# Kernel optimization log

Hardware: AMD Instinct MI355X
Metric: run time of the kernel (lower is better)

## Reference

```python
import jax, jax.numpy as jnp
import numpy as np

C_Z = 128
C_HIDDEN = 128
N_RES = 384
B = 1
EPS = 1e-5


def _layernorm(x, w, b):
    mu = jnp.mean(x, axis=-1, keepdims=True)
    var = jnp.mean(jnp.square(x - mu), axis=-1, keepdims=True)
    return (x - mu) * jax.lax.rsqrt(var + EPS) * w + b


def setup_inputs() -> dict:
    key = jax.random.key(0)
    ks = jax.random.split(key, 16)
    s_z = 1.0 / np.sqrt(C_Z)
    s_h = 1.0 / np.sqrt(C_HIDDEN)
    return {
        "z": jax.random.normal(ks[0], (B, N_RES, N_RES, C_Z), dtype=jnp.float32),
        "mask": jnp.ones((B, N_RES, N_RES), dtype=jnp.float32),
        "ln_in_w": jnp.ones((C_Z,), jnp.float32),
        "ln_in_b": jnp.zeros((C_Z,), jnp.float32),
        "a_g_w": jax.random.normal(ks[1], (C_HIDDEN, C_Z), jnp.float32) * s_z,
        "a_g_b": jnp.zeros((C_HIDDEN,), jnp.float32),
        "a_p_w": jax.random.normal(ks[2], (C_HIDDEN, C_Z), jnp.float32) * s_z,
        "a_p_b": jnp.zeros((C_HIDDEN,), jnp.float32),
        "b_g_w": jax.random.normal(ks[3], (C_HIDDEN, C_Z), jnp.float32) * s_z,
        "b_g_b": jnp.zeros((C_HIDDEN,), jnp.float32),
        "b_p_w": jax.random.normal(ks[4], (C_HIDDEN, C_Z), jnp.float32) * s_z,
        "b_p_b": jnp.zeros((C_HIDDEN,), jnp.float32),
        "g_w": jax.random.normal(ks[5], (C_Z, C_Z), jnp.float32) * s_z,
        "g_b": jnp.zeros((C_Z,), jnp.float32),
        "ln_out_w": jnp.ones((C_HIDDEN,), jnp.float32),
        "ln_out_b": jnp.zeros((C_HIDDEN,), jnp.float32),
        "z_w": jax.random.normal(ks[6], (C_Z, C_HIDDEN), jnp.float32) * s_h,
        "z_b": jnp.zeros((C_Z,), jnp.float32),
    }


def reference(z, mask, ln_in_w, ln_in_b, a_g_w, a_g_b, a_p_w, a_p_b,
              b_g_w, b_g_b, b_p_w, b_p_b, g_w, g_b,
              ln_out_w, ln_out_b, z_w, z_b):
    # z: [B, N, N, c_z]; mask: [B, N, N]
    m = mask[..., None]
    zn = _layernorm(z, ln_in_w, ln_in_b)
    # gated projections (fused LN+GEMM+sigmoid*mul in the Triton kernel)
    a = m * jax.nn.sigmoid(jnp.einsum("bijc,hc->bijh", zn, a_g_w) + a_g_b) \
          * (jnp.einsum("bijc,hc->bijh", zn, a_p_w) + a_p_b)
    b = m * jax.nn.sigmoid(jnp.einsum("bijc,hc->bijh", zn, b_g_w) + b_g_b) \
          * (jnp.einsum("bijc,hc->bijh", zn, b_p_w) + b_p_b)
    # outgoing triangle update: contract over third node k, per channel
    x = jnp.einsum("bikh,bjkh->bijh", a, b)
    # output path: sigmoid(gate(zn)) * linear_z(LN_out(x))
    xn = _layernorm(x, ln_out_w, ln_out_b)
    gate = jax.nn.sigmoid(jnp.einsum("bijc,oc->bijo", zn, g_w) + g_b)
    out = gate * (jnp.einsum("bijh,oh->bijo", xn, z_w) + z_b)
    return out
```

## Files before the change

kernel.cpp:

```cpp
#include <hip/hip_runtime.h>

#define NRES 384
#define CD   128
#define MTOT (NRES*NRES)

typedef unsigned short u16;
typedef __bf16 bf16x8 __attribute__((ext_vector_type(8)));
typedef float  f32x16 __attribute__((ext_vector_type(16)));

static __device__ __forceinline__ u16 f2bf(float f) {
  __bf16 b = (__bf16)f;
  return __builtin_bit_cast(u16, b);
}
static __device__ __forceinline__ float bf2f(u16 v) {
  return __uint_as_float(((unsigned)v) << 16);
}
static __device__ __forceinline__ float sigmoidf(float x) {
  return 1.0f / (1.0f + __expf(-x));
}

__global__ void k_cvt_w(const float* w0, const float* w1, const float* w2,
                        const float* w3, const float* w4, const float* w5,
                        u16* wb) {
  int i = blockIdx.x * 256 + threadIdx.x;
  const float* srcs[6] = {w0, w1, w2, w3, w4, w5};
  wb[i] = f2bf(srcs[i >> 14][i & 16383]);
}

__global__ __launch_bounds__(256) void k_ln_in(const float* __restrict__ z,
                                               const float* __restrict__ w,
                                               const float* __restrict__ b,
                                               u16* __restrict__ zn) {
  int wv = threadIdx.x >> 6, lane = threadIdx.x & 63;
  float2 wv2 = ((const float2*)w)[lane];
  float2 bv2 = ((const float2*)b)[lane];
  for (int rr = 0; rr < 4; ++rr) {
    size_t row = (size_t)blockIdx.x * 16 + wv * 4 + rr;
    float2 v = ((const float2*)(z + row * CD))[lane];
    float s = v.x + v.y;
#pragma unroll
    for (int off = 32; off >= 1; off >>= 1) s += __shfl_xor(s, off);
    float mu = s * (1.0f / CD);
    float dx = v.x - mu, dy = v.y - mu;
    float vr = dx * dx + dy * dy;
#pragma unroll
    for (int off = 32; off >= 1; off >>= 1) vr += __shfl_xor(vr, off);
    float rs = rsqrtf(vr * (1.0f / CD) + 1e-5f);
    ushort2 o;
    o.x = f2bf(dx * rs * wv2.x + bv2.x);
    o.y = f2bf(dy * rs * wv2.y + bv2.y);
    ((ushort2*)(zn + row * CD))[lane] = o;
  }
}

__global__ __launch_bounds__(256) void k_proj(
    const u16* __restrict__ zn, const float* __restrict__ mask,
    const u16* __restrict__ wb,
    const float* __restrict__ agb, const float* __restrict__ apb,
    const float* __restrict__ bgb, const float* __restrict__ bpb,
    const float* __restrict__ gb,
    u16* __restrict__ a_out, u16* __restrict__ b_out, u16* __restrict__ gate_out) {
  int type = blockIdx.y;
  int m0   = blockIdx.x * 64;
  int wv = threadIdx.x >> 6, lane = threadIdx.x & 63;
  int nl = lane & 31, s = lane >> 5;
  int h = wv * 32 + nl;

  const u16 *wgp, *wpp = nullptr;
  const float *bgp, *bpp = nullptr;
  if (type == 0)      { wgp = wb;          wpp = wb + 16384; bgp = agb; bpp = apb; }
  else if (type == 1) { wgp = wb + 32768;  wpp = wb + 49152; bgp = bgb; bpp = bpb; }
  else                { wgp = wb + 65536;                    bgp = gb; }

  __shared__ u16 znt[64][136];

#pragma unroll
  for (int it = 0; it < 4; ++it) {
    int idx = it * 256 + threadIdx.x;
    int r = idx >> 4, c8 = idx & 15;
    *(uint4*)&znt[r][c8 * 8] =
        *(const uint4*)(zn + (size_t)(m0 + r) * CD + c8 * 8);
  }

  bf16x8 wgf[8], wpf[8];
#pragma unroll
  for (int kk = 0; kk < 8; ++kk) {
    wgf[kk] = *(const bf16x8*)(wgp + h * CD + kk * 16 + s * 8);
    if (type < 2) wpf[kk] = *(const bf16x8*)(wpp + h * CD + kk * 16 + s * 8);
  }
  __syncthreads();

  if (type < 2) {
    f32x16 accg[2], accp[2];
#pragma unroll
    for (int i = 0; i < 16; ++i) { accg[0][i] = 0; accg[1][i] = 0; accp[0][i] = 0; accp[1][i] = 0; }
#pragma unroll
    for (int kk = 0; kk < 8; ++kk) {
      bf16x8 zf0 = *(const bf16x8*)&znt[nl][kk * 16 + s * 8];
      bf16x8 zf1 = *(const bf16x8*)&znt[32 + nl][kk * 16 + s * 8];
      accg[0] = __builtin_amdgcn_mfma_f32_32x32x16_bf16(wgf[kk], zf0, accg[0], 0, 0, 0);
      accg[1] = __builtin_amdgcn_mfma_f32_32x32x16_bf16(wgf[kk], zf1, accg[1], 0, 0, 0);
      accp[0] = __builtin_amdgcn_mfma_f32_32x32x16_bf16(wpf[kk], zf0, accp[0], 0, 0, 0);
      accp[1] = __builtin_amdgcn_mfma_f32_32x32x16_bf16(wpf[kk], zf1, accp[1], 0, 0, 0);
    }
    float mk0 = mask[m0 + nl];
    float mk1 = mask[m0 + 32 + nl];
    u16* outp = (type == 0) ? a_out : b_out;
#pragma unroll
    for (int r = 0; r < 16; ++r) {
      int hh = wv * 32 + (r & 3) + 8 * (r >> 2) + 4 * s;
      float bg = bgp[hh], bp = bpp[hh];
      u16* rowp = outp + (size_t)hh * MTOT + m0 + nl;
      rowp[0]  = f2bf(mk0 * sigmoidf(accg[0][r] + bg) * (accp[0][r] + bp));
      rowp[32] = f2bf(mk1 * sigmoidf(accg[1][r] + bg) * (accp[1][r] + bp));
    }
  } else {
    f32x16 accg[2];
#pragma unroll
    for (int i = 0; i < 16; ++i) { accg[0][i] = 0; accg[1][i] = 0; }
#pragma unroll
    for (int kk = 0; kk < 8; ++kk) {
      bf16x8 zf0 = *(const bf16x8*)&znt[nl][kk * 16 + s * 8];
      bf16x8 zf1 = *(const bf16x8*)&znt[32 + nl][kk * 16 + s * 8];
      accg[0] = __builtin_amdgcn_mfma_f32_32x32x16_bf16(zf0, wgf[kk], accg[0], 0, 0, 0);
      accg[1] = __builtin_amdgcn_mfma_f32_32x32x16_bf16(zf1, wgf[kk], accg[1], 0, 0, 0);
    }
    float bgv = bgp[h];
#pragma unroll
    for (int ms = 0; ms < 2; ++ms)
#pragma unroll
      for (int r = 0; r < 16; ++r) {
        int rowoff = (r & 3) + 8 * (r >> 2) + 4 * s;
        int mg = m0 + ms * 32 + rowoff;
        gate_out[(size_t)mg * CD + h] = f2bf(sigmoidf(accg[ms][r] + bgv));
      }
  }
}

__global__ __launch_bounds__(256) void k_tri(const u16* __restrict__ a,
                                             const u16* __restrict__ b,
                                             u16* __restrict__ x) {
  int h  = blockIdx.y;
  int tm = blockIdx.x / 3, tn = blockIdx.x % 3;
  int i0 = tm * 128, j0 = tn * 128;
  const u16* ah = a + (size_t)h * MTOT;
  const u16* bh = b + (size_t)h * MTOT;

  __shared__ u16 At[128][72];
  __shared__ u16 Bt[128][72];

  int wv = threadIdx.x >> 6, lane = threadIdx.x & 63;
  int nl = lane & 31, s = lane >> 5;
  int wr = wv >> 1, wc = wv & 1;

  f32x16 acc[4];
#pragma unroll
  for (int q = 0; q < 4; ++q)
#pragma unroll
    for (int i = 0; i < 16; ++i) acc[q][i] = 0;

  for (int k0 = 0; k0 < NRES; k0 += 64) {
#pragma unroll
    for (int it = 0; it < 4; ++it) {
      int idx = it * 256 + threadIdx.x;
      int r = idx >> 3, c8 = idx & 7;
      *(uint4*)&At[r][c8 * 8] =
          *(const uint4*)(ah + (size_t)(i0 + r) * NRES + k0 + c8 * 8);
    }
#pragma unroll
    for (int it = 0; it < 4; ++it) {
      int idx = it * 256 + threadIdx.x;
      int r = idx >> 3, c8 = idx & 7;
      *(uint4*)&Bt[r][c8 * 8] =
          *(const uint4*)(bh + (size_t)(j0 + r) * NRES + k0 + c8 * 8);
    }
    __syncthreads();
#pragma unroll
    for (int kk = 0; kk < 4; ++kk) {
      bf16x8 af0 = *(const bf16x8*)&At[wr * 64 + nl][kk * 16 + s * 8];
      bf16x8 af1 = *(const bf16x8*)&At[wr * 64 + 32 + nl][kk * 16 + s * 8];
      bf16x8 bf0 = *(const bf16x8*)&Bt[wc * 64 + nl][kk * 16 + s * 8];
      bf16x8 bf1 = *(const bf16x8*)&Bt[wc * 64 + 32 + nl][kk * 16 + s * 8];
      acc[0] = __builtin_amdgcn_mfma_f32_32x32x16_bf16(af0, bf0, acc[0], 0, 0, 0);
      acc[1] = __builtin_amdgcn_mfma_f32_32x32x16_bf16(af0, bf1, acc[1], 0, 0, 0);
      acc[2] = __builtin_amdgcn_mfma_f32_32x32x16_bf16(af1, bf0, acc[2], 0, 0, 0);
      acc[3] = __builtin_amdgcn_mfma_f32_32x32x16_bf16(af1, bf1, acc[3], 0, 0, 0);
    }
    __syncthreads();
  }

  u16* xh = x + (size_t)h * MTOT;
#pragma unroll
  for (int msub = 0; msub < 2; ++msub)
#pragma unroll
    for (int nsub = 0; nsub < 2; ++nsub) {
      int j = j0 + wc * 64 + nsub * 32 + nl;
#pragma unroll
      for (int r = 0; r < 16; ++r) {
        int i = i0 + wr * 64 + msub * 32 + (r & 3) + 8 * (r >> 2) + 4 * s;
        xh[(size_t)i * NRES + j] = f2bf(acc[msub * 2 + nsub][r]);
      }
    }
}

__global__ __launch_bounds__(256) void k_out(
    const u16* __restrict__ x, const u16* __restrict__ gate,
    const u16* __restrict__ wb,
    const float* __restrict__ lnw, const float* __restrict__ lnb,
    const float* __restrict__ zb, float* __restrict__ out) {
  int m0 = blockIdx.x * 64;
  int t = threadIdx.x;
  int wv = t >> 6, lane = t & 63, nl = lane & 31, s = lane >> 5;
  int o = wv * 32 + nl;

  __shared__ u16 xnt[64][136];

  const u16* zwp = wb + 5 * 16384;
  bf16x8 zwf[8];
#pragma unroll
  for (int kk = 0; kk < 8; ++kk)
    zwf[kk] = *(const bf16x8*)(zwp + o * CD + kk * 16 + s * 8);

#pragma unroll
  for (int ps = 0; ps < 2; ++ps) {
    int idx = ps * 256 + t;
    int hp = idx >> 3, mc = idx & 7;
    uint4 v0 = *(const uint4*)(x + (size_t)(2 * hp)     * MTOT + m0 + mc * 8);
    uint4 v1 = *(const uint4*)(x + (size_t)(2 * hp + 1) * MTOT + m0 + mc * 8);
    unsigned c0[4] = {v0.x, v0.y, v0.z, v0.w};
    unsigned c1[4] = {v1.x, v1.y, v1.z, v1.w};
#pragma unroll
    for (int q = 0; q < 4; ++q) {
      ushort2 lo, hi;
      lo.x = (u16)(c0[q] & 0xffffu); lo.y = (u16)(c1[q] & 0xffffu);
      hi.x = (u16)(c0[q] >> 16);     hi.y = (u16)(c1[q] >> 16);
      *(ushort2*)&xnt[mc * 8 + 2 * q][2 * hp]     = lo;
      *(ushort2*)&xnt[mc * 8 + 2 * q + 1][2 * hp] = hi;
    }
  }
  __syncthreads();

  int r = t >> 2, q = t & 3;
  float vals[32];
  float sum = 0;
#pragma unroll
  for (int j = 0; j < 32; ++j) { float v = bf2f(xnt[r][q * 32 + j]); vals[j] = v; sum += v; }
  sum += __shfl_xor(sum, 1);
  sum += __shfl_xor(sum, 2);
  float mu = sum * (1.0f / CD);
  float var = 0;
#pragma unroll
  for (int j = 0; j < 32; ++j) { float d = vals[j] - mu; var += d * d; }
  var += __shfl_xor(var, 1);
  var += __shfl_xor(var, 2);
  float rs = rsqrtf(var * (1.0f / CD) + 1e-5f);
#pragma unroll
  for (int j = 0; j < 32; ++j) {
    int hh = q * 32 + j;
    xnt[r][hh] = f2bf((vals[j] - mu) * rs * lnw[hh] + lnb[hh]);
  }
  __syncthreads();

  f32x16 acc[2];
#pragma unroll
  for (int i = 0; i < 16; ++i) { acc[0][i] = 0; acc[1][i] = 0; }
#pragma unroll
  for (int kk = 0; kk < 8; ++kk) {
    bf16x8 af0 = *(const bf16x8*)&xnt[nl][kk * 16 + s * 8];
    bf16x8 af1 = *(const bf16x8*)&xnt[32 + nl][kk * 16 + s * 8];
    acc[0] = __builtin_amdgcn_mfma_f32_32x32x16_bf16(af0, zwf[kk], acc[0], 0, 0, 0);
    acc[1] = __builtin_amdgcn_mfma_f32_32x32x16_bf16(af1, zwf[kk], acc[1], 0, 0, 0);
  }

  float zbv = zb[o];
#pragma unroll
  for (int ms = 0; ms < 2; ++ms)
#pragma unroll
    for (int rr = 0; rr < 16; ++rr) {
      int rowoff = (rr & 3) + 8 * (rr >> 2) + 4 * s;
      int mg = m0 + ms * 32 + rowoff;
      float g = bf2f(gate[(size_t)mg * CD + o]);
      out[(size_t)mg * CD + o] = g * (acc[ms][rr] + zbv);
    }
}

extern "C" void kernel_launch(void* const* d_in, const int* in_sizes, int n_in,
                              void* d_out, int out_size, void* d_ws, size_t ws_size,
                              hipStream_t stream) {
  const float* z       = (const float*)d_in[0];
  const float* mask    = (const float*)d_in[1];
  const float* ln_in_w = (const float*)d_in[2];
  const float* ln_in_b = (const float*)d_in[3];
  const float* a_g_w   = (const float*)d_in[4];
  const float* a_g_b   = (const float*)d_in[5];
  const float* a_p_w   = (const float*)d_in[6];
  const float* a_p_b   = (const float*)d_in[7];
  const float* b_g_w   = (const float*)d_in[8];
  const float* b_g_b   = (const float*)d_in[9];
  const float* b_p_w   = (const float*)d_in[10];
  const float* b_p_b   = (const float*)d_in[11];
  const float* g_w     = (const float*)d_in[12];
  const float* g_b     = (const float*)d_in[13];
  const float* ln_o_w  = (const float*)d_in[14];
  const float* ln_o_b  = (const float*)d_in[15];
  const float* z_w     = (const float*)d_in[16];
  const float* z_b     = (const float*)d_in[17];
  float* out = (float*)d_out;

  const size_t SZ = (size_t)MTOT * CD * sizeof(u16);
  char* w = (char*)d_ws;
  u16* zn   = (u16*)(w);
  u16* a    = (u16*)(w + SZ);
  u16* b    = (u16*)(w + 2 * SZ);
  u16* gate = (u16*)(w + 3 * SZ);
  u16* wb   = (u16*)(w + 4 * SZ);
  (void)ws_size; (void)in_sizes; (void)n_in; (void)out_size;

  k_cvt_w<<<384, 256, 0, stream>>>(a_g_w, a_p_w, b_g_w, b_p_w, g_w, z_w, wb);
  k_ln_in<<<MTOT / 16, 256, 0, stream>>>(z, ln_in_w, ln_in_b, zn);
  k_proj<<<dim3(MTOT / 64, 3), 256, 0, stream>>>(zn, mask, wb,
      a_g_b, a_p_b, b_g_b, b_p_b, g_b, a, b, gate);
  k_tri<<<dim3(9, 128), 256, 0, stream>>>(a, b, zn);
  k_out<<<MTOT / 64, 256, 0, stream>>>(zn, gate, wb, ln_o_w, ln_o_b, z_b, out);
}
```

Measured before the change: 316.1 us.

## Use direct global-to-LDS loads with XOR swizzle and double-buffered projection tiles

k_proj now covers four 64-row tiles per block, reusing the weight fragments held in registers. It double-buffers the zn tile in LDS, loading it with global_load_lds so the next tile's fetch overlaps the current MFMA work. k_tri also switches to global_load_lds with an XOR-swizzled, unpadded LDS layout in place of the register round-trip and padding. The intent is less VGPR staging traffic, fewer LDS bank conflicts and amortised weight loads. The cost is a quarter as many k_proj blocks, and synchronisation correctness now depends on the asynchronous LDS loads having completed before each barrier.

```diff
diff --git a/kernel.cpp b/kernel.cpp
--- a/kernel.cpp
+++ b/kernel.cpp
@@ -17,6 +17,12 @@
 }
 static __device__ __forceinline__ float sigmoidf(float x) {
   return 1.0f / (1.0f + __expf(-x));
+}
+
+static __device__ __forceinline__ void gl16(const void* g, void* l) {
+  __builtin_amdgcn_global_load_lds(
+      (const __attribute__((address_space(1))) void*)g,
+      (__attribute__((address_space(3))) void*)l, 16, 0, 0);
 }
 
 __global__ void k_cvt_w(const float* w0, const float* w1, const float* w2,
@@ -61,10 +67,11 @@
     const float* __restrict__ gb,
     u16* __restrict__ a_out, u16* __restrict__ b_out, u16* __restrict__ gate_out) {
   int type = blockIdx.y;
-  int m0   = blockIdx.x * 64;
-  int wv = threadIdx.x >> 6, lane = threadIdx.x & 63;
+  int m_base = blockIdx.x * 256;
+  int lane = threadIdx.x & 63;
+  int wvu = __builtin_amdgcn_readfirstlane(threadIdx.x >> 6);
   int nl = lane & 31, s = lane >> 5;
-  int h = wv * 32 + nl;
+  int h = wvu * 32 + nl;
 
   const u16 *wgp, *wpp = nullptr;
   const float *bgp, *bpp = nullptr;
@@ -72,15 +79,7 @@
   else if (type == 1) { wgp = wb + 32768;  wpp = wb + 49152; bgp = bgb; bpp = bpb; }
   else                { wgp = wb + 65536;                    bgp = gb; }
 
-  __shared__ u16 znt[64][136];
-
-#pragma unroll
-  for (int it = 0; it < 4; ++it) {
-    int idx = it * 256 + threadIdx.x;
-    int r = idx >> 4, c8 = idx & 15;
-    *(uint4*)&znt[r][c8 * 8] =
-        *(const uint4*)(zn + (size_t)(m0 + r) * CD + c8 * 8);
-  }
+  __shared__ u16 znt[2][64][128];
 
   bf16x8 wgf[8], wpf[8];
 #pragma unroll
@@ -88,53 +87,77 @@
     wgf[kk] = *(const bf16x8*)(wgp + h * CD + kk * 16 + s * 8);
     if (type < 2) wpf[kk] = *(const bf16x8*)(wpp + h * CD + kk * 16 + s * 8);
   }
+
+  int rl = lane >> 4, p16 = lane & 15;
+#define STAGE_ZNT(mt, bf)                                                   \
+  {                                                                         \
+    _Pragma("unroll")                                                       \
+    for (int j = 0; j < 4; ++j) {                                           \
+      int row = wvu * 16 + j * 4 + rl;                                      \
+      int gc = (p16 ^ (row & 7)) << 3;                                      \
+      gl16(zn + (size_t)((mt) + row) * CD + gc, &znt[bf][wvu * 16 + j * 4][0]); \
+    }                                                                       \
+  }
+
+  STAGE_ZNT(m_base, 0);
   __syncthreads();
 
-  if (type < 2) {
-    f32x16 accg[2], accp[2];
-#pragma unroll
-    for (int i = 0; i < 16; ++i) { accg[0][i] = 0; accg[1][i] = 0; accp[0][i] = 0; accp[1][i] = 0; }
-#pragma unroll
-    for (int kk = 0; kk < 8; ++kk) {
-      bf16x8 zf0 = *(const bf16x8*)&znt[nl][kk * 16 + s * 8];
-      bf16x8 zf1 = *(const bf16x8*)&znt[32 + nl][kk * 16 + s * 8];
-      accg[0] = __builtin_amdgcn_mfma_f32_32x32x16_bf16(wgf[kk], zf0, accg[0], 0, 0, 0);
-      accg[1] = __builtin_amdgcn_mfma_f32_32x32x16_bf16(wgf[kk], zf1, accg[1], 0, 0, 0);
-      accp[0] = __builtin_amdgcn_mfma_f32_32x32x16_bf16(wpf[kk], zf0, accp[0], 0, 0, 0);
-      accp[1] = __builtin_amdgcn_mfma_f32_32x32x16_bf16(wpf[kk], zf1, accp[1], 0, 0, 0);
-    }
-    float mk0 = mask[m0 + nl];
-    float mk1 = mask[m0 + 32 + nl];
-    u16* outp = (type == 0) ? a_out : b_out;
-#pragma unroll
-    for (int r = 0; r < 16; ++r) {
-      int hh = wv * 32 + (r & 3) + 8 * (r >> 2) + 4 * s;
-      float bg = bgp[hh], bp = bpp[hh];
-      u16* rowp = outp + (size_t)hh * MTOT + m0 + nl;
-      rowp[0]  = f2bf(mk0 * sigmoidf(accg[0][r] + bg) * (accp[0][r] + bp));
-      rowp[32] = f2bf(mk1 * sigmoidf(accg[1][r] + bg) * (accp[1][r] + bp));
-    }
-  } else {
-    f32x16 accg[2];
-#pragma unroll
-    for (int i = 0; i < 16; ++i) { accg[0][i] = 0; accg[1][i] = 0; }
-#pragma unroll
-    for (int kk = 0; kk < 8; ++kk) {
-      bf16x8 zf0 = *(const bf16x8*)&znt[nl][kk * 16 + s * 8];
-      bf16x8 zf1 = *(const bf16x8*)&znt[32 + nl][kk * 16 + s * 8];
-      accg[0] = __builtin_amdgcn_mfma_f32_32x32x16_bf16(zf0, wgf[kk], accg[0], 0, 0, 0);
-      accg[1] = __builtin_amdgcn_mfma_f32_32x32x16_bf16(zf1, wgf[kk], accg[1], 0, 0, 0);
-    }
-    float bgv = bgp[h];
-#pragma unroll
-    for (int ms = 0; ms < 2; ++ms)
+  for (int ms = 0; ms < 4; ++ms) {
+    int cur = ms & 1;
+    if (ms < 3) STAGE_ZNT(m_base + (ms + 1) * 64, cur ^ 1);
+    int mt = m_base + ms * 64;
+
+    if (type < 2) {
+      f32x16 accg[2], accp[2];
+#pragma unroll
+      for (int i = 0; i < 16; ++i) { accg[0][i] = 0; accg[1][i] = 0; accp[0][i] = 0; accp[1][i] = 0; }
+#pragma unroll
+      for (int kk = 0; kk < 8; ++kk) {
+        int c = ((kk * 2 + s) ^ (nl & 7)) << 3;
+        bf16x8 zf0 = *(const bf16x8*)&znt[cur][nl][c];
+        bf16x8 zf1 = *(const bf16x8*)&znt[cur][32 + nl][c];
+        accg[0] = __builtin_amdgcn_mfma_f32_32x32x16_bf16(wgf[kk], zf0, accg[0], 0, 0, 0);
+        accg[1] = __builtin_amdgcn_mfma_f32_32x32x16_bf16(wgf[kk], zf1, accg[1], 0, 0, 0);
+        accp[0] = __builtin_amdgcn_mfma_f32_32x32x16_bf16(wpf[kk], zf0, accp[0], 0, 0, 0);
+        accp[1] = __builtin_amdgcn_mfma_f32_32x32x16_bf16(wpf[kk], zf1, accp[1], 0, 0, 0);
+      }
+      __syncthreads();
+      float mk0 = mask[mt + nl];
+      float mk1 = mask[mt + 32 + nl];
+      u16* outp = (type == 0) ? a_out : b_out;
 #pragma unroll
       for (int r = 0; r < 16; ++r) {
-        int rowoff = (r & 3) + 8 * (r >> 2) + 4 * s;
-        int mg = m0 + ms * 32 + rowoff;
-        gate_out[(size_t)mg * CD + h] = f2bf(sigmoidf(accg[ms][r] + bgv));
+        int hh = wvu * 32 + (r & 3) + 8 * (r >> 2) + 4 * s;
+        float bg = bgp[hh], bp = bpp[hh];
+        u16* rowp = outp + (size_t)hh * MTOT + mt + nl;
+        rowp[0]  = f2bf(mk0 * sigmoidf(accg[0][r] + bg) * (accp[0][r] + bp));
+        rowp[32] = f2bf(mk1 * sigmoidf(accg[1][r] + bg) * (accp[1][r] + bp));
       }
-  }
+    } else {
+      f32x16 accg[2];
+#pragma unroll
+      for (int i = 0; i < 16; ++i) { accg[0][i] = 0; accg[1][i] = 0; }
+#pragma unroll
+      for (int kk = 0; kk < 8; ++kk) {
+        int c = ((kk * 2 + s) ^ (nl & 7)) << 3;
+        bf16x8 zf0 = *(const bf16x8*)&znt[cur][nl][c];
+        bf16x8 zf1 = *(const bf16x8*)&znt[cur][32 + nl][c];
+        accg[0] = __builtin_amdgcn_mfma_f32_32x32x16_bf16(zf0, wgf[kk], accg[0], 0, 0, 0);
+        accg[1] = __builtin_amdgcn_mfma_f32_32x32x16_bf16(zf1, wgf[kk], accg[1], 0, 0, 0);
+      }
+      __syncthreads();
+      float bgv = bgp[h];
+#pragma unroll
+      for (int msb = 0; msb < 2; ++msb)
+#pragma unroll
+        for (int r = 0; r < 16; ++r) {
+          int rowoff = (r & 3) + 8 * (r >> 2) + 4 * s;
+          int mg = mt + msb * 32 + rowoff;
+          gate_out[(size_t)mg * CD + h] = f2bf(sigmoidf(accg[msb][r] + bgv));
+        }
+    }
+  }
+#undef STAGE_ZNT
 }
 
 __global__ __launch_bounds__(256) void k_tri(const u16* __restrict__ a,
@@ -146,12 +169,14 @@
   const u16* ah = a + (size_t)h * MTOT;
   const u16* bh = b + (size_t)h * MTOT;
 
-  __shared__ u16 At[128][72];
-  __shared__ u16 Bt[128][72];
-
-  int wv = threadIdx.x >> 6, lane = threadIdx.x & 63;
+  __shared__ u16 At[128][64];
+  __shared__ u16 Bt[128][64];
+
+  int lane = threadIdx.x & 63;
+  int wvu = __builtin_amdgcn_readfirstlane(threadIdx.x >> 6);
   int nl = lane & 31, s = lane >> 5;
-  int wr = wv >> 1, wc = wv & 1;
+  int wr = wvu >> 1, wc = wvu & 1;
+  int rl = lane >> 3, p8 = lane & 7;
 
   f32x16 acc[4];
 #pragma unroll
@@ -161,26 +186,20 @@
 
   for (int k0 = 0; k0 < NRES; k0 += 64) {
 #pragma unroll
-    for (int it = 0; it < 4; ++it) {
-      int idx = it * 256 + threadIdx.x;
-      int r = idx >> 3, c8 = idx & 7;
-      *(uint4*)&At[r][c8 * 8] =
-          *(const uint4*)(ah + (size_t)(i0 + r) * NRES + k0 + c8 * 8);
-    }
-#pragma unroll
-    for (int it = 0; it < 4; ++it) {
-      int idx = it * 256 + threadIdx.x;
-      int r = idx >> 3, c8 = idx & 7;
-      *(uint4*)&Bt[r][c8 * 8] =
-          *(const uint4*)(bh + (size_t)(j0 + r) * NRES + k0 + c8 * 8);
+    for (int j = 0; j < 4; ++j) {
+      int row = wvu * 32 + j * 8 + rl;
+      int gc = (p8 ^ (rl & 7)) << 3;
+      gl16(ah + (size_t)(i0 + row) * NRES + k0 + gc, &At[wvu * 32 + j * 8][0]);
+      gl16(bh + (size_t)(j0 + row) * NRES + k0 + gc, &Bt[wvu * 32 + j * 8][0]);
     }
     __syncthreads();
 #pragma unroll
     for (int kk = 0; kk < 4; ++kk) {
-      bf16x8 af0 = *(const bf16x8*)&At[wr * 64 + nl][kk * 16 + s * 8];
-      bf16x8 af1 = *(const bf16x8*)&At[wr * 64 + 32 + nl][kk * 16 + s * 8];
-      bf16x8 bf0 = *(const bf16x8*)&Bt[wc * 64 + nl][kk * 16 + s * 8];
-      bf16x8 bf1 = *(const bf16x8*)&Bt[wc * 64 + 32 + nl][kk * 16 + s * 8];
+      int c = ((kk * 2 + s) ^ (nl & 7)) << 3;
+      bf16x8 af0 = *(const bf16x8*)&At[wr * 64 + nl][c];
+      bf16x8 af1 = *(const bf16x8*)&At[wr * 64 + 32 + nl][c];
+      bf16x8 bf0 = *(const bf16x8*)&Bt[wc * 64 + nl][c];
+      bf16x8 bf1 = *(const bf16x8*)&Bt[wc * 64 + 32 + nl][c];
       acc[0] = __builtin_amdgcn_mfma_f32_32x32x16_bf16(af0, bf0, acc[0], 0, 0, 0);
       acc[1] = __builtin_amdgcn_mfma_f32_32x32x16_bf16(af0, bf1, acc[1], 0, 0, 0);
       acc[2] = __builtin_amdgcn_mfma_f32_32x32x16_bf16(af1, bf0, acc[2], 0, 0, 0);
@@ -318,7 +337,7 @@
 
   k_cvt_w<<<384, 256, 0, stream>>>(a_g_w, a_p_w, b_g_w, b_p_w, g_w, z_w, wb);
   k_ln_in<<<MTOT / 16, 256, 0, stream>>>(z, ln_in_w, ln_in_b, zn);
-  k_proj<<<dim3(MTOT / 64, 3), 256, 0, stream>>>(zn, mask, wb,
+  k_proj<<<dim3(MTOT / 256, 3), 256, 0, stream>>>(zn, mask, wb,
       a_g_b, a_p_b, b_g_b, b_p_b, g_b, a, b, gate);
   k_tri<<<dim3(9, 128), 256, 0, stream>>>(a, b, zn);
   k_out<<<MTOT / 64, 256, 0, stream>>>(zn, gate, wb, ln_o_w, ln_o_b, z_b, out);
```

Result: faster. 299.9 us (-5.1%).
